# Optimization experiments

Measured on AMD Instinct MI355X. Metric: run time of the kernel, lower is better.

Reference implementation:

```python
import jax, jax.numpy as jnp
import numpy as np
import math

B, E, K, H, NH = 8, 256, 64, 768, 12
HD = H // NH


def setup_inputs() -> dict:
    key = jax.random.key(0)
    ks = jax.random.split(key, 10)
    s = 0.02
    return {
        "q_in": jax.random.normal(ks[0], (B, E, 1, H), jnp.float32),
        "k_in": jax.random.normal(ks[1], (B, E, K, H), jnp.float32),
        "v_in": jax.random.normal(ks[2], (B, E, K, H), jnp.float32),
        "type_score": jax.random.uniform(ks[3], (B, E, 1, 1, K), jnp.float32),
        "Wq": jax.random.normal(ks[4], (H, H), jnp.float32) * s,
        "bq": jnp.zeros((H,), jnp.float32),
        "Wk": jax.random.normal(ks[5], (H, H), jnp.float32) * s,
        "bk": jnp.zeros((H,), jnp.float32),
        "Wv": jax.random.normal(ks[6], (H, H), jnp.float32) * s,
        "bv": jnp.zeros((H,), jnp.float32),
    }


def _heads(x):
    # [B,E,S,H] -> [B,E,nh,S,hd]
    b, e, s, _ = x.shape
    return x.reshape(b, e, s, NH, HD).transpose(0, 1, 3, 2, 4)


def reference(q_in, k_in, v_in, type_score, Wq, bq, Wk, bk, Wv, bv):
    q = _heads(q_in @ Wq.T + bq)   # [B,E,nh,1,hd]
    k = _heads(k_in @ Wk.T + bk)   # [B,E,nh,K,hd]
    v = _heads(v_in @ Wv.T + bv)   # [B,E,nh,K,hd]
    scores = jnp.einsum('behqd,behkd->behqk', q, k) / math.sqrt(HD)
    probs = jax.nn.softmax(scores, axis=-1)
    # post-softmax type reweighting (dropout = identity in eval)
    probs = probs * type_score
    ctx = jnp.einsum('behqk,behkd->behqd', probs, v)   # [B,E,nh,1,hd]
    ctx = ctx.transpose(0, 1, 3, 2, 4).reshape(B, E, 1, H)
    return ctx.squeeze(-2)  # [B,E,H]
```

## Files before the change

kernel.cpp:

```cpp
#include <hip/hip_runtime.h>
#include <stdint.h>

#define Bdim  8
#define Edim  256
#define Kdim  64
#define Hdim  768
#define NHdim 12
#define HDdim 64

typedef __attribute__((ext_vector_type(8))) short short8;
typedef __attribute__((ext_vector_type(4))) float floatx4;
typedef unsigned short ushort_t;
typedef unsigned int u32;

#define GPLANE (2048*768)

__device__ __forceinline__ float bf2f(ushort_t u){
  union { u32 i; float f; } v; v.i = ((u32)u) << 16; return v.f;
}
__device__ __forceinline__ ushort_t f2bf(float f){
  union { float f; u32 i; } v; v.f = f;
  u32 r = v.i + 0x7fffu + ((v.i >> 16) & 1u);
  return (ushort_t)(r >> 16);
}

__device__ __forceinline__ void async_ld16(void* lds, const void* g){
  __builtin_amdgcn_global_load_lds(
      (const __attribute__((address_space(1))) u32*)(uintptr_t)g,
      (__attribute__((address_space(3))) u32*)(u32)(uintptr_t)lds,
      16, 0, 0);
}

template<int STORE_BF16>
__global__ __launch_bounds__(256, 2)
void gemm_proj(const float* __restrict__ A, const ushort_t* __restrict__ W,
               const float* __restrict__ bias, void* __restrict__ Cout)
{
  __shared__ __align__(16) char smem[34816];
  const int t    = threadIdx.x;
  const int lane = t & 63;
  const int wave = t >> 6;
  const int wm   = wave >> 1, wn = wave & 1;
  const int n0   = blockIdx.x * 128;
  const int m0   = blockIdx.y * 128;

  floatx4 acc[4][4];
#pragma unroll
  for (int i = 0; i < 4; i++)
#pragma unroll
    for (int j = 0; j < 4; j++) acc[i][j] = (floatx4)0.f;

  int am[4], ac[4];
#pragma unroll
  for (int q = 0; q < 4; q++){ int idx = q*256 + t; am[q] = idx >> 3; ac[q] = idx & 7; }

  float4 areg[4];
  const int NT = Hdim / 32;

  char* const smemc = (char*)smem;
  auto Abase = [&](int b){ return smemc + b*16384; };
  auto Wbase = [&](int b){ return smemc + b*16384 + 8192; };

  auto loadA = [&](int kt){
    const float* Ap = A + (size_t)m0*768 + kt*32;
#pragma unroll
    for (int q = 0; q < 4; q++)
      areg[q] = *(const float4*)(Ap + (size_t)am[q]*768 + ac[q]*4);
  };
  auto writeA = [&](int b){
    char* base = Abase(b);
#pragma unroll
    for (int q = 0; q < 4; q++){
      u32 lo = (u32)f2bf(areg[q].x) | ((u32)f2bf(areg[q].y) << 16);
      u32 hi = (u32)f2bf(areg[q].z) | ((u32)f2bf(areg[q].w) << 16);
      int off = am[q]*64 + ((ac[q]*8) ^ ((am[q]&3) << 4));
      u32* p = (u32*)(base + off);
      p[0] = lo; p[1] = hi;
    }
  };
  auto stageW = [&](int kt, int b){
    char* base = Wbase(b);
#pragma unroll
    for (int i = 0; i < 2; i++){
      int s  = i*256 + t;
      int n  = s >> 2, kc = s & 3;
      int kcs = kc ^ (n & 3);
      const ushort_t* g = W + (size_t)(n0 + n)*768 + kt*32 + kcs*8;
      char* ldst = base + (i*256 + wave*64) * 16;
      async_ld16(ldst, g);
    }
  };
  auto compute = [&](int b){
    char* ab = Abase(b);
    char* wb = Wbase(b);
    short8 af[4], bf[4];
#pragma unroll
    for (int mi = 0; mi < 4; mi++){
      int row = wm*64 + mi*16 + (lane & 15);
      int off = row*64 + (((lane >> 4) * 16) ^ ((row & 3) << 4));
      af[mi] = *(const short8*)(ab + off);
    }
#pragma unroll
    for (int ni = 0; ni < 4; ni++){
      int row = wn*64 + ni*16 + (lane & 15);
      int off = row*64 + (((lane >> 4) * 16) ^ ((row & 3) << 4));
      bf[ni] = *(const short8*)(wb + off);
    }
#pragma unroll
    for (int mi = 0; mi < 4; mi++)
#pragma unroll
      for (int ni = 0; ni < 4; ni++)
        acc[mi][ni] = __builtin_amdgcn_mfma_f32_16x16x32_bf16(af[mi], bf[ni], acc[mi][ni], 0, 0, 0);
  };

  int buf = 0;
  loadA(0);
  stageW(0, 0);
  writeA(0);
  asm volatile("s_waitcnt vmcnt(0)" ::: "memory");
  __syncthreads();

  for (int kt = 0; kt < NT; ++kt){
    if (kt + 1 < NT){
      loadA(kt + 1);
      stageW(kt + 1, buf ^ 1);
    }
    compute(buf);
    if (kt + 1 < NT) writeA(buf ^ 1);
    asm volatile("s_waitcnt vmcnt(0)" ::: "memory");
    __syncthreads();
    buf ^= 1;
  }

  float bvv[4];
#pragma unroll
  for (int ni = 0; ni < 4; ni++) bvv[ni] = bias[n0 + wn*64 + ni*16 + (lane & 15)];

  if (STORE_BF16){
    ushort_t* sc = (ushort_t*)smem;
#pragma unroll
    for (int mi = 0; mi < 4; mi++){
      int row0 = wm*64 + mi*16 + ((lane >> 4) << 2);
#pragma unroll
      for (int ni = 0; ni < 4; ni++){
        int col = wn*64 + ni*16 + (lane & 15);
#pragma unroll
        for (int r = 0; r < 4; r++)
          sc[(row0 + r)*136 + col] = f2bf(acc[mi][ni][r] + bvv[ni]);
      }
    }
    __syncthreads();
    ushort_t* C = (ushort_t*)Cout;
    int row = t >> 1, seg = t & 1;
    const char* src = smemc + row*272 + seg*128;
    char* dst = (char*)(C + (size_t)(m0 + row)*768 + n0 + seg*64);
#pragma unroll
    for (int c = 0; c < 8; c++)
      *(floatx4*)(dst + c*16) = *(const floatx4*)(src + c*16);
  } else {
    float* C = (float*)Cout;
#pragma unroll
    for (int mi = 0; mi < 4; mi++){
      int row0 = wm*64 + mi*16 + ((lane >> 4) << 2);
#pragma unroll
      for (int ni = 0; ni < 4; ni++){
        int col = wn*64 + ni*16 + (lane & 15);
#pragma unroll
        for (int r = 0; r < 4; r++)
          C[(size_t)(m0 + row0 + r)*768 + n0 + col] = acc[mi][ni][r] + bvv[ni];
      }
    }
  }
}

__global__ __launch_bounds__(256)
void cvt_w(const float* __restrict__ W, ushort_t* __restrict__ O)
{
  int i = (blockIdx.x * 256 + threadIdx.x) * 4;
  float4 v = *(const float4*)(W + i);
  u32 lo = (u32)f2bf(v.x) | ((u32)f2bf(v.y) << 16);
  u32 hi = (u32)f2bf(v.z) | ((u32)f2bf(v.w) << 16);
  u32* p = (u32*)(O + i);
  p[0] = lo; p[1] = hi;
}

__global__ __launch_bounds__(256)
void cvt_wT(const float* __restrict__ W, ushort_t* __restrict__ O)
{
  __shared__ float tile[32][33];
  int bo = blockIdx.x * 32;
  int bc = blockIdx.y * 32;
  int tx = threadIdx.x & 31, ty = threadIdx.x >> 5;
#pragma unroll
  for (int i = 0; i < 4; i++)
    tile[ty + 8*i][tx] = W[(size_t)(bo + ty + 8*i)*768 + bc + tx];
  __syncthreads();
#pragma unroll
  for (int i = 0; i < 4; i++)
    O[(size_t)(bc + ty + 8*i)*768 + bo + tx] = f2bf(tile[tx][ty + 8*i]);
}

__global__ __launch_bounds__(256)
void gemm_g(const ushort_t* __restrict__ qp, const ushort_t* __restrict__ WkT,
            ushort_t* __restrict__ g)
{
  const int h  = blockIdx.z;
  const int n0 = blockIdx.x * 128;
  const int m0 = blockIdx.y * 128;
  const int t = threadIdx.x, lane = t & 63, wave = t >> 6;
  const int wm = wave >> 1, wn = wave & 1;
  const int hl = lane & 15, jr = lane >> 4;

  floatx4 acc[4][4];
#pragma unroll
  for (int i = 0; i < 4; i++)
#pragma unroll
    for (int j = 0; j < 4; j++) acc[i][j] = (floatx4)0.f;

#pragma unroll
  for (int kt = 0; kt < 2; kt++){
    short8 af[4], bf[4];
#pragma unroll
    for (int mi = 0; mi < 4; mi++)
      af[mi] = *(const short8*)(qp + (size_t)(m0 + wm*64 + mi*16 + hl)*768 + h*64 + kt*32 + jr*8);
#pragma unroll
    for (int ni = 0; ni < 4; ni++)
      bf[ni] = *(const short8*)(WkT + (size_t)(n0 + wn*64 + ni*16 + hl)*768 + h*64 + kt*32 + jr*8);
#pragma unroll
    for (int mi = 0; mi < 4; mi++)
#pragma unroll
      for (int ni = 0; ni < 4; ni++)
        acc[mi][ni] = __builtin_amdgcn_mfma_f32_16x16x32_bf16(af[mi], bf[ni], acc[mi][ni], 0, 0, 0);
  }

  ushort_t* gp = g + (size_t)h * GPLANE;
#pragma unroll
  for (int mi = 0; mi < 4; mi++){
#pragma unroll
    for (int ni = 0; ni < 4; ni++){
      int col = n0 + wn*64 + ni*16 + hl;
#pragma unroll
      for (int r = 0; r < 4; r++){
        int row = m0 + wm*64 + mi*16 + jr*4 + r;
        gp[(size_t)row*768 + col] = f2bf(acc[mi][ni][r]);
      }
    }
  }
}

__global__ __launch_bounds__(256)
void attn_scores(const float* __restrict__ k_in, const float* __restrict__ tsc,
                 const ushort_t* __restrict__ g, float* __restrict__ probs)
{
  const int be = blockIdx.x;
  const int t = threadIdx.x, lane = t & 63, w = t >> 6;
  const int hl = lane & 15, jr = lane >> 4;

  __shared__ float redmax[4][16];
  __shared__ float redsum[4][16];

  const float* krow = k_in + (size_t)be*Kdim*768 + (size_t)(w*16 + hl)*768;
  const int hq = (hl < 12) ? hl : 0;
  const ushort_t* grow = g + (size_t)hq*GPLANE + (size_t)be*768;

  floatx4 acc = (floatx4)0.f;
#pragma unroll 4
  for (int kt = 0; kt < 24; kt++){
    int c0 = kt*32 + jr*8;
    float4 f0 = *(const float4*)(krow + c0);
    float4 f1 = *(const float4*)(krow + c0 + 4);
    short8 af;
    af[0]=(short)f2bf(f0.x); af[1]=(short)f2bf(f0.y); af[2]=(short)f2bf(f0.z); af[3]=(short)f2bf(f0.w);
    af[4]=(short)f2bf(f1.x); af[5]=(short)f2bf(f1.y); af[6]=(short)f2bf(f1.z); af[7]=(short)f2bf(f1.w);
    short8 bf = *(const short8*)(grow + c0);
    acc = __builtin_amdgcn_mfma_f32_16x16x32_bf16(af, bf, acc, 0, 0, 0);
  }

  float s[4];
#pragma unroll
  for (int r = 0; r < 4; r++) s[r] = acc[r] * 0.125f;

  float wmax = fmaxf(fmaxf(s[0], s[1]), fmaxf(s[2], s[3]));
  wmax = fmaxf(wmax, __shfl_xor(wmax, 16));
  wmax = fmaxf(wmax, __shfl_xor(wmax, 32));
  if (jr == 0) redmax[w][hl] = wmax;
  __syncthreads();
  float gm = fmaxf(fmaxf(redmax[0][hl], redmax[1][hl]),
                   fmaxf(redmax[2][hl], redmax[3][hl]));

  float e[4], es = 0.f;
#pragma unroll
  for (int r = 0; r < 4; r++){ e[r] = __expf(s[r] - gm); es += e[r]; }
  es += __shfl_xor(es, 16);
  es += __shfl_xor(es, 32);
  if (jr == 0) redsum[w][hl] = es;
  __syncthreads();
  float S = redsum[0][hl] + redsum[1][hl] + redsum[2][hl] + redsum[3][hl];
  float invS = 1.0f / S;

  float4 t4 = *(const float4*)(tsc + be*64 + w*16 + jr*4);
  if (hl < 12){
    float4 pv = make_float4(e[0]*invS*t4.x, e[1]*invS*t4.y,
                            e[2]*invS*t4.z, e[3]*invS*t4.w);
    *(float4*)(probs + (size_t)be*768 + hl*64 + w*16 + jr*4) = pv;
  }
}

__global__ __launch_bounds__(384)
void attn_u(const float* __restrict__ v_in, const float* __restrict__ probs,
            ushort_t* __restrict__ Ug, float* __restrict__ ps_g)
{
  const int be = blockIdx.x;
  const int t = threadIdx.x;

  __shared__ float P[12][64];

  ((float*)P)[t]       = probs[(size_t)be*768 + t];
  ((float*)P)[t + 384] = probs[(size_t)be*768 + t + 384];
  __syncthreads();

  if (t < 12){
    float s = 0.f;
#pragma unroll
    for (int jb = 0; jb < 16; jb++){
      float4 p4 = *(const float4*)&P[t][jb*4];
      s += p4.x + p4.y + p4.z + p4.w;
    }
    ps_g[be*12 + t] = s;
  }

  const float* vbase = v_in + (size_t)be*Kdim*768 + 2*t;
  float u0[12], u1[12];
#pragma unroll
  for (int h = 0; h < 12; h++){ u0[h] = 0.f; u1[h] = 0.f; }

  for (int jb = 0; jb < 16; jb++){
    float2 v[4];
#pragma unroll
    for (int q = 0; q < 4; q++)
      v[q] = *(const float2*)(vbase + (size_t)(jb*4 + q)*768);
#pragma unroll
    for (int h = 0; h < 12; h++){
      float4 p4 = *(const float4*)&P[h][jb*4];
      u0[h] += p4.x*v[0].x + p4.y*v[1].x + p4.z*v[2].x + p4.w*v[3].x;
      u1[h] += p4.x*v[0].y + p4.y*v[1].y + p4.z*v[2].y + p4.w*v[3].y;
    }
  }

#pragma unroll
  for (int h = 0; h < 12; h++){
    u32 word = (u32)f2bf(u0[h]) | ((u32)f2bf(u1[h]) << 16);
    ((u32*)(Ug + (size_t)h*GPLANE + (size_t)be*768))[t] = word;
  }
}

__global__ __launch_bounds__(256)
void out_proj(const ushort_t* __restrict__ Ug, const ushort_t* __restrict__ Wvb,
              const float* __restrict__ bv, const float* __restrict__ ps_g,
              float* __restrict__ out)
{
  const int h  = blockIdx.y;
  const int m0 = blockIdx.x * 128;
  const int t = threadIdx.x, lane = t & 63, wave = t >> 6;
  const int wm = wave >> 1, wn = wave & 1;
  const int hl = lane & 15, jr = lane >> 4;

  const ushort_t* Up = Ug + (size_t)h*GPLANE;

  floatx4 acc[4][2];
#pragma unroll
  for (int i = 0; i < 4; i++){ acc[i][0] = (floatx4)0.f; acc[i][1] = (floatx4)0.f; }

#pragma unroll 4
  for (int kt = 0; kt < 24; kt++){
    short8 af[4], bf[2];
#pragma unroll
    for (int mi = 0; mi < 4; mi++)
      af[mi] = *(const short8*)(Up + (size_t)(m0 + wm*64 + mi*16 + hl)*768 + kt*32 + jr*8);
#pragma unroll
    for (int ni = 0; ni < 2; ni++)
      bf[ni] = *(const short8*)(Wvb + (size_t)(h*64 + wn*32 + ni*16 + hl)*768 + kt*32 + jr*8);
#pragma unroll
    for (int mi = 0; mi < 4; mi++)
#pragma unroll
      for (int ni = 0; ni < 2; ni++)
        acc[mi][ni] = __builtin_amdgcn_mfma_f32_16x16x32_bf16(af[mi], bf[ni], acc[mi][ni], 0, 0, 0);
  }

  float bvo[2];
#pragma unroll
  for (int ni = 0; ni < 2; ni++) bvo[ni] = bv[h*64 + wn*32 + ni*16 + hl];

#pragma unroll
  for (int mi = 0; mi < 4; mi++){
#pragma unroll
    for (int r = 0; r < 4; r++){
      int be = m0 + wm*64 + mi*16 + jr*4 + r;
      float psv = ps_g[be*12 + h];
#pragma unroll
      for (int ni = 0; ni < 2; ni++)
        out[(size_t)be*768 + h*64 + wn*32 + ni*16 + hl] = acc[mi][ni][r] + bvo[ni]*psv;
    }
  }
}

extern "C" void kernel_launch(void* const* d_in, const int* in_sizes, int n_in,
                              void* d_out, int out_size, void* d_ws, size_t ws_size,
                              hipStream_t stream)
{
  const float* q_in = (const float*)d_in[0];
  const float* k_in = (const float*)d_in[1];
  const float* v_in = (const float*)d_in[2];
  const float* tsc  = (const float*)d_in[3];
  const float* Wq   = (const float*)d_in[4];
  const float* bq   = (const float*)d_in[5];
  const float* Wk   = (const float*)d_in[6];
  const float* Wv   = (const float*)d_in[8];
  const float* bv   = (const float*)d_in[9];

  char* ws = (char*)d_ws;
  ushort_t* Wqb  = (ushort_t*)(ws);
  ushort_t* Wvb  = (ushort_t*)(ws + 1179648);
  ushort_t* WkTb = (ushort_t*)(ws + 2359296);
  ushort_t* qp   = (ushort_t*)(ws + 3538944);
  ushort_t* g    = (ushort_t*)(ws + 6684672);
  ushort_t* Ug   = (ushort_t*)(ws + 44433408);
  float*    ps_g = (float*)   (ws + 82182144);
  float*    probs= (float*)   (ws + 82280448);

  cvt_w <<<576, 256, 0, stream>>>(Wq, Wqb);
  cvt_w <<<576, 256, 0, stream>>>(Wv, Wvb);
  cvt_wT<<<dim3(24, 24), 256, 0, stream>>>(Wk, WkTb);

  gemm_proj<1><<<dim3(6, 16), 256, 0, stream>>>(q_in, Wqb, bq, (void*)qp);

  gemm_g<<<dim3(6, 16, 12), 256, 0, stream>>>(qp, WkTb, g);

  attn_scores<<<2048, 256, 0, stream>>>(k_in, tsc, g, probs);

  attn_u<<<2048, 384, 0, stream>>>(v_in, probs, Ug, ps_g);

  out_proj<<<dim3(16, 12), 256, 0, stream>>>(Ug, Wvb, bv, ps_g, (float*)d_out);
}
```

Measured before the change: 269.7 us.

## Fuse score softmax with value reduction and merge weight conversion launches

Merges the attention-score kernel and the value-weighting kernel into one 384-thread kernel. The first four waves compute softmax probabilities into shared memory, and all waves then reduce the value rows, so the global probs buffer round trip and one launch go away. The three weight conversion kernels are folded into a single prep launch, and scalar bf16 rounding is replaced with the packed v_cvt_pk_bf16_f32 instruction. In exchange, two of the six waves sit idle during the score phase, and the larger block may reduce occupancy.

```diff
diff --git a/kernel.cpp b/kernel.cpp
--- a/kernel.cpp
+++ b/kernel.cpp
@@ -23,6 +23,11 @@
   u32 r = v.i + 0x7fffu + ((v.i >> 16) & 1u);
   return (ushort_t)(r >> 16);
 }
+__device__ __forceinline__ u32 cvtpk(float lo, float hi){
+  u32 r;
+  asm("v_cvt_pk_bf16_f32 %0, %1, %2" : "=v"(r) : "v"(lo), "v"(hi));
+  return r;
+}
 
 __device__ __forceinline__ void async_ld16(void* lds, const void* g){
   __builtin_amdgcn_global_load_lds(
@@ -31,10 +36,9 @@
       16, 0, 0);
 }
 
-template<int STORE_BF16>
 __global__ __launch_bounds__(256, 2)
 void gemm_proj(const float* __restrict__ A, const ushort_t* __restrict__ W,
-               const float* __restrict__ bias, void* __restrict__ Cout)
+               const float* __restrict__ bias, ushort_t* __restrict__ Cout)
 {
   __shared__ __align__(16) char smem[34816];
   const int t    = threadIdx.x;
@@ -136,68 +140,56 @@
 #pragma unroll
   for (int ni = 0; ni < 4; ni++) bvv[ni] = bias[n0 + wn*64 + ni*16 + (lane & 15)];
 
-  if (STORE_BF16){
-    ushort_t* sc = (ushort_t*)smem;
-#pragma unroll
-    for (int mi = 0; mi < 4; mi++){
-      int row0 = wm*64 + mi*16 + ((lane >> 4) << 2);
-#pragma unroll
-      for (int ni = 0; ni < 4; ni++){
-        int col = wn*64 + ni*16 + (lane & 15);
-#pragma unroll
-        for (int r = 0; r < 4; r++)
-          sc[(row0 + r)*136 + col] = f2bf(acc[mi][ni][r] + bvv[ni]);
-      }
-    }
+  ushort_t* sc = (ushort_t*)smem;
+#pragma unroll
+  for (int mi = 0; mi < 4; mi++){
+    int row0 = wm*64 + mi*16 + ((lane >> 4) << 2);
+#pragma unroll
+    for (int ni = 0; ni < 4; ni++){
+      int col = wn*64 + ni*16 + (lane & 15);
+#pragma unroll
+      for (int r = 0; r < 4; r++)
+        sc[(row0 + r)*136 + col] = f2bf(acc[mi][ni][r] + bvv[ni]);
+    }
+  }
+  __syncthreads();
+  int row = t >> 1, seg = t & 1;
+  const char* src = smemc + row*272 + seg*128;
+  char* dst = (char*)(Cout + (size_t)(m0 + row)*768 + n0 + seg*64);
+#pragma unroll
+  for (int c = 0; c < 8; c++)
+    *(floatx4*)(dst + c*16) = *(const floatx4*)(src + c*16);
+}
+
+__global__ __launch_bounds__(256)
+void prep(const float* __restrict__ Wq, const float* __restrict__ Wv,
+          const float* __restrict__ Wk, ushort_t* __restrict__ Wqb,
+          ushort_t* __restrict__ Wvb, ushort_t* __restrict__ WkTb)
+{
+  __shared__ float tile[32][33];
+  const int b = blockIdx.x;
+  if (b < 1152){
+    const float* src = (b < 576) ? Wq : Wv;
+    ushort_t*    dst = (b < 576) ? Wqb : Wvb;
+    int bb = (b < 576) ? b : b - 576;
+    int i = (bb * 256 + threadIdx.x) * 4;
+    float4 v = *(const float4*)(src + i);
+    u32* p = (u32*)(dst + i);
+    p[0] = (u32)f2bf(v.x) | ((u32)f2bf(v.y) << 16);
+    p[1] = (u32)f2bf(v.z) | ((u32)f2bf(v.w) << 16);
+  } else {
+    int bb = b - 1152;
+    int bo = (bb / 24) * 32;
+    int bc = (bb % 24) * 32;
+    int tx = threadIdx.x & 31, ty = threadIdx.x >> 5;
+#pragma unroll
+    for (int i = 0; i < 4; i++)
+      tile[ty + 8*i][tx] = Wk[(size_t)(bo + ty + 8*i)*768 + bc + tx];
     __syncthreads();
-    ushort_t* C = (ushort_t*)Cout;
-    int row = t >> 1, seg = t & 1;
-    const char* src = smemc + row*272 + seg*128;
-    char* dst = (char*)(C + (size_t)(m0 + row)*768 + n0 + seg*64);
-#pragma unroll
-    for (int c = 0; c < 8; c++)
-      *(floatx4*)(dst + c*16) = *(const floatx4*)(src + c*16);
-  } else {
-    float* C = (float*)Cout;
-#pragma unroll
-    for (int mi = 0; mi < 4; mi++){
-      int row0 = wm*64 + mi*16 + ((lane >> 4) << 2);
-#pragma unroll
-      for (int ni = 0; ni < 4; ni++){
-        int col = wn*64 + ni*16 + (lane & 15);
-#pragma unroll
-        for (int r = 0; r < 4; r++)
-          C[(size_t)(m0 + row0 + r)*768 + n0 + col] = acc[mi][ni][r] + bvv[ni];
-      }
-    }
-  }
-}
-
-__global__ __launch_bounds__(256)
-void cvt_w(const float* __restrict__ W, ushort_t* __restrict__ O)
-{
-  int i = (blockIdx.x * 256 + threadIdx.x) * 4;
-  float4 v = *(const float4*)(W + i);
-  u32 lo = (u32)f2bf(v.x) | ((u32)f2bf(v.y) << 16);
-  u32 hi = (u32)f2bf(v.z) | ((u32)f2bf(v.w) << 16);
-  u32* p = (u32*)(O + i);
-  p[0] = lo; p[1] = hi;
-}
-
-__global__ __launch_bounds__(256)
-void cvt_wT(const float* __restrict__ W, ushort_t* __restrict__ O)
-{
-  __shared__ float tile[32][33];
-  int bo = blockIdx.x * 32;
-  int bc = blockIdx.y * 32;
-  int tx = threadIdx.x & 31, ty = threadIdx.x >> 5;
-#pragma unroll
-  for (int i = 0; i < 4; i++)
-    tile[ty + 8*i][tx] = W[(size_t)(bo + ty + 8*i)*768 + bc + tx];
-  __syncthreads();
-#pragma unroll
-  for (int i = 0; i < 4; i++)
-    O[(size_t)(bc + ty + 8*i)*768 + bo + tx] = f2bf(tile[tx][ty + 8*i]);
+#pragma unroll
+    for (int i = 0; i < 4; i++)
+      WkTb[(size_t)(bc + ty + 8*i)*768 + bo + tx] = f2bf(tile[tx][ty + 8*i]);
+  }
 }
 
 __global__ __launch_bounds__(256)
@@ -248,85 +240,77 @@
   }
 }
 
-__global__ __launch_bounds__(256)
-void attn_scores(const float* __restrict__ k_in, const float* __restrict__ tsc,
-                 const ushort_t* __restrict__ g, float* __restrict__ probs)
+__global__ __launch_bounds__(384)
+void attn_main(const float* __restrict__ k_in, const float* __restrict__ v_in,
+               const float* __restrict__ tsc, const ushort_t* __restrict__ g,
+               ushort_t* __restrict__ Ug, float* __restrict__ ps_g)
 {
   const int be = blockIdx.x;
   const int t = threadIdx.x, lane = t & 63, w = t >> 6;
   const int hl = lane & 15, jr = lane >> 4;
 
+  __shared__ float P[12][64];
   __shared__ float redmax[4][16];
   __shared__ float redsum[4][16];
 
-  const float* krow = k_in + (size_t)be*Kdim*768 + (size_t)(w*16 + hl)*768;
-  const int hq = (hl < 12) ? hl : 0;
-  const ushort_t* grow = g + (size_t)hq*GPLANE + (size_t)be*768;
-
-  floatx4 acc = (floatx4)0.f;
+  float s[4], e[4], gm;
+  if (w < 4){
+    const float* krow = k_in + (size_t)be*Kdim*768 + (size_t)(w*16 + hl)*768;
+    const int hq = (hl < 12) ? hl : 0;
+    const ushort_t* grow = g + (size_t)hq*GPLANE + (size_t)be*768;
+
+    floatx4 acc = (floatx4)0.f;
 #pragma unroll 4
-  for (int kt = 0; kt < 24; kt++){
-    int c0 = kt*32 + jr*8;
-    float4 f0 = *(const float4*)(krow + c0);
-    float4 f1 = *(const float4*)(krow + c0 + 4);
-    short8 af;
-    af[0]=(short)f2bf(f0.x); af[1]=(short)f2bf(f0.y); af[2]=(short)f2bf(f0.z); af[3]=(short)f2bf(f0.w);
-    af[4]=(short)f2bf(f1.x); af[5]=(short)f2bf(f1.y); af[6]=(short)f2bf(f1.z); af[7]=(short)f2bf(f1.w);
-    short8 bf = *(const short8*)(grow + c0);
-    acc = __builtin_amdgcn_mfma_f32_16x16x32_bf16(af, bf, acc, 0, 0, 0);
-  }
-
-  float s[4];
-#pragma unroll
-  for (int r = 0; r < 4; r++) s[r] = acc[r] * 0.125f;
-
-  float wmax = fmaxf(fmaxf(s[0], s[1]), fmaxf(s[2], s[3]));
-  wmax = fmaxf(wmax, __shfl_xor(wmax, 16));
-  wmax = fmaxf(wmax, __shfl_xor(wmax, 32));
-  if (jr == 0) redmax[w][hl] = wmax;
+    for (int kt = 0; kt < 24; kt++){
+      int c0 = kt*32 + jr*8;
+      float4 f0 = *(const float4*)(krow + c0);
+      float4 f1 = *(const float4*)(krow + c0 + 4);
+      union { short8 s8; u32 wd[4]; } A;
+      A.wd[0] = cvtpk(f0.x, f0.y);
+      A.wd[1] = cvtpk(f0.z, f0.w);
+      A.wd[2] = cvtpk(f1.x, f1.y);
+      A.wd[3] = cvtpk(f1.z, f1.w);
+      short8 bf = *(const short8*)(grow + c0);
+      acc = __builtin_amdgcn_mfma_f32_16x16x32_bf16(A.s8, bf, acc, 0, 0, 0);
+    }
+#pragma unroll
+    for (int r = 0; r < 4; r++) s[r] = acc[r] * 0.125f;
+
+    float wmax = fmaxf(fmaxf(s[0], s[1]), fmaxf(s[2], s[3]));
+    wmax = fmaxf(wmax, __shfl_xor(wmax, 16));
+    wmax = fmaxf(wmax, __shfl_xor(wmax, 32));
+    if (jr == 0) redmax[w][hl] = wmax;
+  }
   __syncthreads();
-  float gm = fmaxf(fmaxf(redmax[0][hl], redmax[1][hl]),
-                   fmaxf(redmax[2][hl], redmax[3][hl]));
-
-  float e[4], es = 0.f;
-#pragma unroll
-  for (int r = 0; r < 4; r++){ e[r] = __expf(s[r] - gm); es += e[r]; }
-  es += __shfl_xor(es, 16);
-  es += __shfl_xor(es, 32);
-  if (jr == 0) redsum[w][hl] = es;
+  if (w < 4){
+    gm = fmaxf(fmaxf(redmax[0][hl], redmax[1][hl]),
+               fmaxf(redmax[2][hl], redmax[3][hl]));
+    float es = 0.f;
+#pragma unroll
+    for (int r = 0; r < 4; r++){ e[r] = __expf(s[r] - gm); es += e[r]; }
+    es += __shfl_xor(es, 16);
+    es += __shfl_xor(es, 32);
+    if (jr == 0) redsum[w][hl] = es;
+  }
   __syncthreads();
-  float S = redsum[0][hl] + redsum[1][hl] + redsum[2][hl] + redsum[3][hl];
-  float invS = 1.0f / S;
-
-  float4 t4 = *(const float4*)(tsc + be*64 + w*16 + jr*4);
-  if (hl < 12){
+  if (w < 4 && hl < 12){
+    float S = redsum[0][hl] + redsum[1][hl] + redsum[2][hl] + redsum[3][hl];
+    float invS = 1.0f / S;
+    float4 t4 = *(const float4*)(tsc + be*64 + w*16 + jr*4);
     float4 pv = make_float4(e[0]*invS*t4.x, e[1]*invS*t4.y,
                             e[2]*invS*t4.z, e[3]*invS*t4.w);
-    *(float4*)(probs + (size_t)be*768 + hl*64 + w*16 + jr*4) = pv;
-  }
-}
-
-__global__ __launch_bounds__(384)
-void attn_u(const float* __restrict__ v_in, const float* __restrict__ probs,
-            ushort_t* __restrict__ Ug, float* __restrict__ ps_g)
-{
-  const int be = blockIdx.x;
-  const int t = threadIdx.x;
-
-  __shared__ float P[12][64];
-
-  ((float*)P)[t]       = probs[(size_t)be*768 + t];
-  ((float*)P)[t + 384] = probs[(size_t)be*768 + t + 384];
+    *(float4*)&P[hl][w*16 + jr*4] = pv;
+  }
   __syncthreads();
 
   if (t < 12){
-    float s = 0.f;
+    float sum = 0.f;
 #pragma unroll
     for (int jb = 0; jb < 16; jb++){
       float4 p4 = *(const float4*)&P[t][jb*4];
-      s += p4.x + p4.y + p4.z + p4.w;
-    }
-    ps_g[be*12 + t] = s;
+      sum += p4.x + p4.y + p4.z + p4.w;
+    }
+    ps_g[be*12 + t] = sum;
   }
 
   const float* vbase = v_in + (size_t)be*Kdim*768 + 2*t;
@@ -348,10 +332,8 @@
   }
 
 #pragma unroll
-  for (int h = 0; h < 12; h++){
-    u32 word = (u32)f2bf(u0[h]) | ((u32)f2bf(u1[h]) << 16);
-    ((u32*)(Ug + (size_t)h*GPLANE + (size_t)be*768))[t] = word;
-  }
+  for (int h = 0; h < 12; h++)
+    ((u32*)(Ug + (size_t)h*GPLANE + (size_t)be*768))[t] = cvtpk(u0[h], u1[h]);
 }
 
 __global__ __launch_bounds__(256)
@@ -426,19 +408,14 @@
   ushort_t* g    = (ushort_t*)(ws + 6684672);
   ushort_t* Ug   = (ushort_t*)(ws + 44433408);
   float*    ps_g = (float*)   (ws + 82182144);
-  float*    probs= (float*)   (ws + 82280448);
-
-  cvt_w <<<576, 256, 0, stream>>>(Wq, Wqb);
-  cvt_w <<<576, 256, 0, stream>>>(Wv, Wvb);
-  cvt_wT<<<dim3(24, 24), 256, 0, stream>>>(Wk, WkTb);
-
-  gemm_proj<1><<<dim3(6, 16), 256, 0, stream>>>(q_in, Wqb, bq, (void*)qp);
+
+  prep<<<1728, 256, 0, stream>>>(Wq, Wv, Wk, Wqb, Wvb, WkTb);
+
+  gemm_proj<<<dim3(6, 16), 256, 0, stream>>>(q_in, Wqb, bq, qp);
 
   gemm_g<<<dim3(6, 16, 12), 256, 0, stream>>>(qp, WkTb, g);
 
-  attn_scores<<<2048, 256, 0, stream>>>(k_in, tsc, g, probs);
-
-  attn_u<<<2048, 384, 0, stream>>>(v_in, probs, Ug, ps_g);
+  attn_main<<<2048, 384, 0, stream>>>(k_in, v_in, tsc, g, Ug, ps_g);
 
   out_proj<<<dim3(16, 12), 256, 0, stream>>>(Ug, Wvb, bv, ps_g, (float*)d_out);
 }
```

After: 268.2 us. No clear change (-0.5%).
